# Kernel tuning notes

Hardware: AMD Instinct MI355X
Metric: run time of the kernel (lower is better)

Reference implementation:

```python
import jax, jax.numpy as jnp
import numpy as np

# Dims / scalars (from init_kwargs: m = int(T/dt), delta = dt, theta_star = threshold)
M = 50000
N = 500
DELTA = 0.001
GLEAK = 1.0
TAUS = 10.0
THETA_STAR = 1.0
SPIKE_PROB = 0.02  # sparse binary spike raster as produced by time2spike


def setup_inputs() -> dict:
    key = jax.random.key(0)
    k1, k2, k3 = jax.random.split(key, 3)
    # binary spike raster [m, n]
    spikes = (jax.random.uniform(k1, (M, N)) < SPIKE_PROB).astype(jnp.float32)
    # synapse weights ~ N(w_mean=0.01, 0.01)
    w = (0.01 + 0.01 * jax.random.normal(k2, (N,))).astype(jnp.float32)
    # reversal potentials: half excitatory (ex=5), half inhibitory (inh=-1), shuffled
    vrev = jnp.where(jax.random.uniform(k3, (N,)) < 0.5, 5.0, -1.0).astype(jnp.float32)
    return {"spikes": spikes, "w": w, "vrev": vrev}


def reference(spikes, w, vrev):
    dtype = spikes.dtype
    decay = jnp.exp(jnp.asarray(-1.0 / TAUS, dtype))

    # _compute_exp: exp_temp[i] = (exp_temp[i-1] + spikes[i-1]) * exp(-1/taus), exp_temp[0] = 0
    def exp_step(carry, s):
        nxt = (carry + s) * decay
        return nxt, nxt

    _, e_tail = jax.lax.scan(exp_step, jnp.zeros((N,), dtype), spikes[:-1])
    exp_temp = jnp.concatenate([jnp.zeros((1, N), dtype), e_tail], axis=0)  # [M, N]

    # Gsyn_pre = |w| * exp_temp ; Isyn_pre = Vrev * |w| * exp_temp.
    # Only their per-timestep sums over synapses enter the vtr recurrence,
    # so contract over n immediately instead of materializing [M, N] products.
    absw = jnp.abs(w)
    g_sum = exp_temp @ absw            # [M] = sum_j Gsyn_pre[i, j]
    i_sum = exp_temp @ (vrev * absw)   # [M] = sum_j Isyn_pre[i, j]
    a = DELTA * (GLEAK + g_sum)        # per-step leak+conductance factor
    b = DELTA * i_sum                  # per-step input drive

    # _computevtr: if vtr[i-1] < theta: vtr[i] = vtr[i-1]*(1 - a[i-1]) + b[i-1]
    # else vtr[i] stays 0 (state reset after threshold crossing), vtr[0] = 0.
    def vtr_step(v, ab):
        ai, bi = ab
        nxt = jnp.where(v < THETA_STAR, v * (1.0 - ai) + bi, jnp.asarray(0.0, dtype))
        return nxt, nxt

    _, v_tail = jax.lax.scan(vtr_step, jnp.asarray(0.0, dtype), (a[:-1], b[:-1]))
    vtr = jnp.concatenate([jnp.zeros((1,), dtype), v_tail])  # [M]
    return vtr
```

## Files before the change

kernel.cpp:

```cpp
#include <hip/hip_runtime.h>
#include <cmath>

namespace {
constexpr int NELEM  = 50000;
constexpr int NSYN   = 500;
constexpr int NQ4    = 125;
constexpr int T      = 1024;
constexpr int SBLK   = 49;
constexpr int SLOTS  = SBLK * T;
constexpr int CMAXC  = (NELEM - 1) >> 6;
constexpr int NCH_PAD = 784;
constexpr int MAXSEG = 4096;
constexpr int NGRP   = NELEM / 8;
constexpr double DELTA_D = 1.0e-3;
constexpr double THETA_D = 1.0;
constexpr float  DECAY_F = 0.90483741803595957311f;
}

struct WS {
    double2 rq[SLOTS];
    double  gAm[64], gAg[64], gAi[64];
    double  gPp[64], gPq[64];
    double  gmaxR[1024];
    double  gbndQ[MAXSEG];
    int     gbnd[MAXSEG];
    int     gnseg;
    int     flagA[64];
    int     flagB[64];
    float   swv[SLOTS];
    float   iwv[SLOTS];
};

__device__ inline void pub_d(double* p, double v) {
    __hip_atomic_store(reinterpret_cast<unsigned long long*>(p),
                       __double_as_longlong(v),
                       __ATOMIC_RELAXED, __HIP_MEMORY_SCOPE_AGENT);
}
__device__ inline double rd_d(const double* p) {
    unsigned long long u =
        __hip_atomic_load(reinterpret_cast<const unsigned long long*>(p),
                          __ATOMIC_RELAXED, __HIP_MEMORY_SCOPE_AGENT);
    return __longlong_as_double(u);
}

__global__ __launch_bounds__(256) void k_rowdot(
    const float* __restrict__ spikes,
    const float* __restrict__ w,
    const float* __restrict__ vrev,
    WS* __restrict__ ws)
{
    if (blockIdx.x == 0 && threadIdx.x < 128) {
        const int l = threadIdx.x;
        if (l < 64) ws->flagA[l] = 0; else ws->flagB[l - 64] = 0;
    }

    const int lane = threadIdx.x & 63;
    const int wv   = threadIdx.x >> 6;
    const int rg   = blockIdx.x * 4 + wv;
    if (rg >= NGRP) return;
    const int row0 = rg * 8;

    const float4* __restrict__ w4 = reinterpret_cast<const float4*>(w);
    const float4* __restrict__ r4 = reinterpret_cast<const float4*>(vrev);
    const int j1 = lane;
    const int j2 = lane + 64;
    const bool has2 = (j2 < NQ4);
    float4 a1 = w4[j1], r1 = r4[j1];
    float4 aw1 = make_float4(fabsf(a1.x), fabsf(a1.y), fabsf(a1.z), fabsf(a1.w));
    float4 ar1 = make_float4(aw1.x * r1.x, aw1.y * r1.y, aw1.z * r1.z, aw1.w * r1.w);
    float4 aw2 = make_float4(0.f, 0.f, 0.f, 0.f), ar2 = aw2;
    if (has2) {
        float4 a2 = w4[j2], r2 = r4[j2];
        aw2 = make_float4(fabsf(a2.x), fabsf(a2.y), fabsf(a2.z), fabsf(a2.w));
        ar2 = make_float4(aw2.x * r2.x, aw2.y * r2.y, aw2.z * r2.z, aw2.w * r2.w);
    }

    float sp[8], ip[8];
#pragma unroll
    for (int r = 0; r < 8; ++r) {
        const float4* __restrict__ srow =
            reinterpret_cast<const float4*>(spikes + (size_t)(row0 + r) * NSYN);
        float4 s1 = srow[j1];
        float a = s1.x * aw1.x + s1.y * aw1.y + s1.z * aw1.z + s1.w * aw1.w;
        float b = s1.x * ar1.x + s1.y * ar1.y + s1.z * ar1.z + s1.w * ar1.w;
        if (has2) {
            float4 s2 = srow[j2];
            a += s2.x * aw2.x + s2.y * aw2.y + s2.z * aw2.z + s2.w * aw2.w;
            b += s2.x * ar2.x + s2.y * ar2.y + s2.z * ar2.z + s2.w * ar2.w;
        }
        sp[r] = a; ip[r] = b;
    }
#pragma unroll
    for (int d = 32; d > 0; d >>= 1) {
#pragma unroll
        for (int r = 0; r < 8; ++r) {
            sp[r] += __shfl_xor(sp[r], d);
            ip[r] += __shfl_xor(ip[r], d);
        }
    }
    if (lane == 0) {
        *reinterpret_cast<float4*>(ws->swv + row0)     = make_float4(sp[0], sp[1], sp[2], sp[3]);
        *reinterpret_cast<float4*>(ws->swv + row0 + 4) = make_float4(sp[4], sp[5], sp[6], sp[7]);
        *reinterpret_cast<float4*>(ws->iwv + row0)     = make_float4(ip[0], ip[1], ip[2], ip[3]);
        *reinterpret_cast<float4*>(ws->iwv + row0 + 4) = make_float4(ip[4], ip[5], ip[6], ip[7]);
    }
}

__global__ __launch_bounds__(1024) void k_scan(WS* __restrict__ ws)
{
    const int tid = threadIdx.x, lane = tid & 63, wv = tid >> 6, blk = blockIdx.x;
    const int idx = blk * T + tid;
    const bool live = (idx < NELEM);
    const double decay = (double)DECAY_F;
    __shared__ double s_a[16], s_b[16], s_c[16];
    __shared__ double s_qg0, s_qi0, s_qp0, s_qq0;

    double s = live ? (double)ws->swv[idx] : 0.0;
    double t = live ? (double)ws->iwv[idx] : 0.0;
    double m_in = live ? decay : 1.0;
    double g_in = live ? s * decay : 0.0;
    double i_in = live ? t * decay : 0.0;
#pragma unroll
    for (int d = 1; d < 64; d <<= 1) {
        double pm = __shfl_up(m_in, d);
        double pg = __shfl_up(g_in, d);
        double pi = __shfl_up(i_in, d);
        if (lane >= d) {
            g_in = m_in * pg + g_in;
            i_in = m_in * pi + i_in;
            m_in = pm * m_in;
        }
    }
    if (lane == 63) { s_a[wv] = m_in; s_b[wv] = g_in; s_c[wv] = i_in; }
    __syncthreads();

    if (wv == 0) {
        double wm = (lane < 16) ? s_a[lane] : 1.0;
        double wg = (lane < 16) ? s_b[lane] : 0.0;
        double wi = (lane < 16) ? s_c[lane] : 0.0;
#pragma unroll
        for (int d = 1; d < 16; d <<= 1) {
            double pm = __shfl_up(wm, d);
            double pg = __shfl_up(wg, d);
            double pi = __shfl_up(wi, d);
            if (lane >= d) {
                wg = wm * pg + wg;
                wi = wm * pi + wi;
                wm = pm * wm;
            }
        }
        if (lane < 16) { s_a[lane] = wm; s_b[lane] = wg; s_c[lane] = wi; }
        if (lane == 15) {
            pub_d(&ws->gAm[blk], wm); pub_d(&ws->gAg[blk], wg); pub_d(&ws->gAi[blk], wi);
            __hip_atomic_store(&ws->flagA[blk], 1, __ATOMIC_RELEASE, __HIP_MEMORY_SCOPE_AGENT);
        }
        double am = 1.0, ag = 0.0, ai = 0.0;
        if (lane < SBLK) {
            while (__hip_atomic_load(&ws->flagA[lane], __ATOMIC_ACQUIRE,
                                     __HIP_MEMORY_SCOPE_AGENT) == 0)
                __builtin_amdgcn_s_sleep(1);
            am = rd_d(&ws->gAm[lane]); ag = rd_d(&ws->gAg[lane]); ai = rd_d(&ws->gAi[lane]);
        }
#pragma unroll
        for (int d = 1; d < 64; d <<= 1) {
            double pm = __shfl_up(am, d);
            double pg = __shfl_up(ag, d);
            double pi = __shfl_up(ai, d);
            if (lane >= d) {
                ag = am * pg + ag;
                ai = am * pi + ai;
                am = pm * am;
            }
        }
        double zg = __shfl_up(ag, 1), zi = __shfl_up(ai, 1);
        if (lane == 0) { zg = 0.0; zi = 0.0; }
        if (lane == blk) { s_qg0 = zg; s_qi0 = zi; }
    }
    __syncthreads();

    double em = __shfl_up(m_in, 1), eg = __shfl_up(g_in, 1), ei = __shfl_up(i_in, 1);
    if (lane == 0) { em = 1.0; eg = 0.0; ei = 0.0; }
    if (wv > 0) {
        double qm = s_a[wv - 1], qg = s_b[wv - 1], qi = s_c[wv - 1];
        eg = em * qg + eg;
        ei = em * qi + ei;
        em = qm * em;
    }
    double Eg = em * s_qg0 + eg;
    double Ei = em * s_qi0 + ei;
    double p_in = 1.0, q_in = 0.0;
    if (live) {
        double aa = DELTA_D * (1.0 + Eg);
        double om = 1.0 - aa;
        p_in = om;
        q_in = (DELTA_D * Ei) / om;
    }
    __syncthreads();

#pragma unroll
    for (int d = 1; d < 64; d <<= 1) {
        double pp = __shfl_up(p_in, d);
        double pq = __shfl_up(q_in, d);
        if (lane >= d) {
            q_in = pq + q_in / pp;
            p_in = pp * p_in;
        }
    }
    if (lane == 63) { s_a[wv] = p_in; s_b[wv] = q_in; }
    __syncthreads();

    if (wv == 0) {
        double wp = (lane < 16) ? s_a[lane] : 1.0;
        double wq = (lane < 16) ? s_b[lane] : 0.0;
#pragma unroll
        for (int d = 1; d < 16; d <<= 1) {
            double pp = __shfl_up(wp, d);
            double pq = __shfl_up(wq, d);
            if (lane >= d) {
                wq = pq + wq / pp;
                wp = pp * wp;
            }
        }
        if (lane < 16) { s_a[lane] = wp; s_b[lane] = wq; }
        if (lane == 15) {
            pub_d(&ws->gPp[blk], wp); pub_d(&ws->gPq[blk], wq);
            __hip_atomic_store(&ws->flagB[blk], 1, __ATOMIC_RELEASE, __HIP_MEMORY_SCOPE_AGENT);
        }
        double ap = 1.0, aq = 0.0;
        if (lane < SBLK) {
            while (__hip_atomic_load(&ws->flagB[lane], __ATOMIC_ACQUIRE,
                                     __HIP_MEMORY_SCOPE_AGENT) == 0)
                __builtin_amdgcn_s_sleep(1);
            ap = rd_d(&ws->gPp[lane]); aq = rd_d(&ws->gPq[lane]);
        }
#pragma unroll
        for (int d = 1; d < 64; d <<= 1) {
            double pp = __shfl_up(ap, d);
            double pq = __shfl_up(aq, d);
            if (lane >= d) {
                aq = pq + aq / pp;
                ap = pp * ap;
            }
        }
        double zp = __shfl_up(ap, 1), zq = __shfl_up(aq, 1);
        if (lane == 0) { zp = 1.0; zq = 0.0; }
        if (lane == blk) { s_qp0 = zp; s_qq0 = zq; }
    }
    __syncthreads();

    double ep = __shfl_up(p_in, 1), eq = __shfl_up(q_in, 1);
    if (lane == 0) { ep = 1.0; eq = 0.0; }
    if (wv > 0) {
        double ap2 = s_a[wv - 1], aq2 = s_b[wv - 1];
        eq = aq2 + eq / ap2;
        ep = ap2 * ep;
    }
    double Q = s_qq0 + eq / s_qp0;
    double P = s_qp0 * ep;
    double R = live ? (Q - THETA_D / P) : -1.0e308;
    ws->rq[idx] = make_double2(R, Q);
    double mR = R;
#pragma unroll
    for (int d = 32; d > 0; d >>= 1) mR = fmax(mR, __shfl_xor(mR, d));
    if (lane == 0) ws->gmaxR[idx >> 6] = mR;
}

__global__ __launch_bounds__(1024) void k_search(WS* __restrict__ ws)
{
    const int tid = threadIdx.x, blk = blockIdx.x;

    if (blk == 0) {
        __shared__ double smax[NCH_PAD];
        for (int c = tid; c < NCH_PAD; c += T)
            smax[c] = (c <= CMAXC) ? ws->gmaxR[c] : -1.0e308;
        __syncthreads();

        if (tid < 64) {
            const int lane = tid;
            int nseg = 1;
            if (lane == 0) { ws->gbnd[0] = 0; ws->gbndQ[0] = 0.0; }
            double Qr = 0.0;
            int pos = 1;
            while (pos < NELEM && nseg < MAXSEG) {
                int c = pos >> 6;
                int i0 = -1;
                double Qnb = 0.0;
                while (true) {
                    int cf = -1;
                    for (int cb = c; cb <= CMAXC; cb += 64) {
                        int cc = cb + lane;
                        bool qy = (cc <= CMAXC) && (smax[cc] >= Qr);
                        unsigned long long m = __ballot(qy);
                        if (m) { cf = cb + __builtin_ctzll(m); break; }
                    }
                    if (cf < 0) break;
                    int i = (cf << 6) + lane;
                    bool valid = (i >= pos) && (i < NELEM);
                    double2 rv = valid ? ws->rq[i] : make_double2(-1.0e308, 0.0);
                    unsigned long long m2 = __ballot(valid && (rv.x >= Qr));
                    if (m2) {
                        int r = __builtin_ctzll(m2);
                        i0 = (cf << 6) + r;
                        if (r < 63) Qnb = __shfl(rv.y, r + 1);
                        break;
                    }
                    c = cf + 1;
                    if (c > CMAXC) break;
                }
                if (i0 < 0) break;
                int nb = i0 + 1;
                if (nb >= NELEM) break;
                if ((i0 & 63) == 63) Qnb = ws->rq[nb].y;
                Qr = Qnb;
                if (lane == 0) { ws->gbnd[nseg] = nb; ws->gbndQ[nseg] = Qr; }
                nseg++;
                pos = nb + 1;
            }
            if (lane == 0) ws->gnseg = nseg;
        } else {
            double acc = 0.0;
            for (int i = tid; i < NELEM; i += 7 * T) acc += ws->rq[i].x;
            asm volatile("" :: "v"((float)acc));
        }
    } else if ((blk & 7) == 0) {
        const int p = blk >> 3;
        double acc = 0.0;
        for (int i = p * T + tid; i < NELEM; i += 7 * T) acc += ws->rq[i].x;
        asm volatile("" :: "v"((float)acc));
    }
}

__global__ __launch_bounds__(1024) void k_fill(const WS* __restrict__ ws,
                                               float* __restrict__ out)
{
    __shared__ int    sb[MAXSEG];
    __shared__ double sq[MAXSEG];
    __shared__ int    s_nseg;
    const int tid = threadIdx.x;
    if (tid == 0) s_nseg = ws->gnseg;
    __syncthreads();
    const int nseg = s_nseg;
    for (int i = tid; i < nseg; i += T) { sb[i] = ws->gbnd[i]; sq[i] = ws->gbndQ[i]; }
    __syncthreads();

    const int idx = blockIdx.x * T + tid;
    if (idx < NELEM) {
        int lo = 0, hi = nseg - 1;
        while (lo < hi) {
            int mid = (lo + hi + 1) >> 1;
            if (sb[mid] <= idx) lo = mid; else hi = mid - 1;
        }
        if (idx == sb[lo]) {
            out[idx] = 0.0f;
        } else {
            double2 v = ws->rq[idx];
            double P = THETA_D / (v.y - v.x);
            out[idx] = (float)(P * (v.y - sq[lo]));
        }
    }
}

extern "C" void kernel_launch(void* const* d_in, const int* in_sizes, int n_in,
                              void* d_out, int out_size, void* d_ws, size_t ws_size,
                              hipStream_t stream) {
    const float* spikes = (const float*)d_in[0];
    const float* w      = (const float*)d_in[1];
    const float* vrev   = (const float*)d_in[2];
    float* out = (float*)d_out;
    WS* ws = (WS*)d_ws;

    hipLaunchKernelGGL(k_rowdot, dim3((NGRP + 3) / 4), dim3(256), 0, stream,
                       spikes, w, vrev, ws);
    hipLaunchKernelGGL(k_scan,   dim3(SBLK), dim3(T), 0, stream, ws);
    hipLaunchKernelGGL(k_search, dim3(56),   dim3(T), 0, stream, ws);
    hipLaunchKernelGGL(k_fill,   dim3(SBLK), dim3(T), 0, stream, ws, out);
}
```

Measured before the change: 194.9 us.

## Fuse search and fill kernels into one launch with flag-based handoff

Merges the serial boundary-search kernel and the output fill kernel into a single kernel. Block 0 runs the search and publishes the segment boundaries with atomic stores and a release flag. Blocks 1..49 preload their rq values, then spin on the flag before doing the binary search and writing output. This removes one kernel launch and its inter-kernel gap, and it repartitions the L2-warming prefetch loops into contiguous shares. The spin-wait assumes block 0 is co-resident with the other blocks; 56 blocks of 1024 threads should fit on the device.

```diff
diff --git a/kernel.cpp b/kernel.cpp
--- a/kernel.cpp
+++ b/kernel.cpp
@@ -12,6 +12,7 @@
 constexpr int NCH_PAD = 784;
 constexpr int MAXSEG = 4096;
 constexpr int NGRP   = NELEM / 8;
+constexpr int PSHARE = 7143;
 constexpr double DELTA_D = 1.0e-3;
 constexpr double THETA_D = 1.0;
 constexpr float  DECAY_F = 0.90483741803595957311f;
@@ -27,6 +28,7 @@
     int     gnseg;
     int     flagA[64];
     int     flagB[64];
+    int     flagS;
     float   swv[SLOTS];
     float   iwv[SLOTS];
 };
@@ -41,6 +43,12 @@
         __hip_atomic_load(reinterpret_cast<const unsigned long long*>(p),
                           __ATOMIC_RELAXED, __HIP_MEMORY_SCOPE_AGENT);
     return __longlong_as_double(u);
+}
+__device__ inline void pub_i(int* p, int v) {
+    __hip_atomic_store(p, v, __ATOMIC_RELAXED, __HIP_MEMORY_SCOPE_AGENT);
+}
+__device__ inline int rd_i(const int* p) {
+    return __hip_atomic_load(p, __ATOMIC_RELAXED, __HIP_MEMORY_SCOPE_AGENT);
 }
 
 __global__ __launch_bounds__(256) void k_rowdot(
@@ -49,9 +57,11 @@
     const float* __restrict__ vrev,
     WS* __restrict__ ws)
 {
-    if (blockIdx.x == 0 && threadIdx.x < 128) {
+    if (blockIdx.x == 0 && threadIdx.x < 129) {
         const int l = threadIdx.x;
-        if (l < 64) ws->flagA[l] = 0; else ws->flagB[l - 64] = 0;
+        if (l < 64) ws->flagA[l] = 0;
+        else if (l < 128) ws->flagB[l - 64] = 0;
+        else ws->flagS = 0;
     }
 
     const int lane = threadIdx.x & 63;
@@ -265,12 +275,15 @@
     if (lane == 0) ws->gmaxR[idx >> 6] = mR;
 }
 
-__global__ __launch_bounds__(1024) void k_search(WS* __restrict__ ws)
+__global__ __launch_bounds__(1024) void k_tail(WS* __restrict__ ws, float* __restrict__ out)
 {
     const int tid = threadIdx.x, blk = blockIdx.x;
+    __shared__ double smax[NCH_PAD];
+    __shared__ int    sb[MAXSEG];
+    __shared__ double sq[MAXSEG];
+    __shared__ int    s_nseg;
 
     if (blk == 0) {
-        __shared__ double smax[NCH_PAD];
         for (int c = tid; c < NCH_PAD; c += T)
             smax[c] = (c <= CMAXC) ? ws->gmaxR[c] : -1.0e308;
         __syncthreads();
@@ -278,7 +291,7 @@
         if (tid < 64) {
             const int lane = tid;
             int nseg = 1;
-            if (lane == 0) { ws->gbnd[0] = 0; ws->gbndQ[0] = 0.0; }
+            if (lane == 0) { pub_i(&ws->gbnd[0], 0); pub_d(&ws->gbndQ[0], 0.0); }
             double Qr = 0.0;
             int pos = 1;
             while (pos < NELEM && nseg < MAXSEG) {
@@ -312,39 +325,50 @@
                 if (nb >= NELEM) break;
                 if ((i0 & 63) == 63) Qnb = ws->rq[nb].y;
                 Qr = Qnb;
-                if (lane == 0) { ws->gbnd[nseg] = nb; ws->gbndQ[nseg] = Qr; }
+                if (lane == 0) { pub_i(&ws->gbnd[nseg], nb); pub_d(&ws->gbndQ[nseg], Qr); }
                 nseg++;
                 pos = nb + 1;
             }
-            if (lane == 0) ws->gnseg = nseg;
+            if (lane == 0) {
+                pub_i(&ws->gnseg, nseg);
+                __hip_atomic_store(&ws->flagS, 1, __ATOMIC_RELEASE, __HIP_MEMORY_SCOPE_AGENT);
+            }
         } else {
             double acc = 0.0;
-            for (int i = tid; i < NELEM; i += 7 * T) acc += ws->rq[i].x;
+            for (int i = tid - 64; i < PSHARE; i += 960) acc += ws->rq[i].x;
             asm volatile("" :: "v"((float)acc));
         }
-    } else if ((blk & 7) == 0) {
+        return;
+    }
+    if (blk > SBLK) return;
+
+    const int st = blk - 1;
+    const int idx = st * T + tid;
+    const bool live = (idx < NELEM);
+    double2 v = live ? ws->rq[idx] : make_double2(0.0, 1.0);
+    asm volatile("" :: "v"(v.x), "v"(v.y));
+
+    if ((blk & 7) == 0) {
         const int p = blk >> 3;
+        const int lo = p * PSHARE;
+        const int hi = (lo + PSHARE < NELEM) ? lo + PSHARE : NELEM;
         double acc = 0.0;
-        for (int i = p * T + tid; i < NELEM; i += 7 * T) acc += ws->rq[i].x;
+        for (int i = lo + tid; i < hi; i += T) acc += ws->rq[i].x;
         asm volatile("" :: "v"((float)acc));
     }
-}
-
-__global__ __launch_bounds__(1024) void k_fill(const WS* __restrict__ ws,
-                                               float* __restrict__ out)
-{
-    __shared__ int    sb[MAXSEG];
-    __shared__ double sq[MAXSEG];
-    __shared__ int    s_nseg;
-    const int tid = threadIdx.x;
-    if (tid == 0) s_nseg = ws->gnseg;
+
+    if (tid == 0) {
+        while (__hip_atomic_load(&ws->flagS, __ATOMIC_ACQUIRE,
+                                 __HIP_MEMORY_SCOPE_AGENT) == 0)
+            __builtin_amdgcn_s_sleep(8);
+        s_nseg = rd_i(&ws->gnseg);
+    }
     __syncthreads();
     const int nseg = s_nseg;
-    for (int i = tid; i < nseg; i += T) { sb[i] = ws->gbnd[i]; sq[i] = ws->gbndQ[i]; }
-    __syncthreads();
-
-    const int idx = blockIdx.x * T + tid;
-    if (idx < NELEM) {
+    for (int i = tid; i < nseg; i += T) { sb[i] = rd_i(&ws->gbnd[i]); sq[i] = rd_d(&ws->gbndQ[i]); }
+    __syncthreads();
+
+    if (live) {
         int lo = 0, hi = nseg - 1;
         while (lo < hi) {
             int mid = (lo + hi + 1) >> 1;
@@ -353,7 +377,6 @@
         if (idx == sb[lo]) {
             out[idx] = 0.0f;
         } else {
-            double2 v = ws->rq[idx];
             double P = THETA_D / (v.y - v.x);
             out[idx] = (float)(P * (v.y - sq[lo]));
         }
@@ -372,6 +395,5 @@
     hipLaunchKernelGGL(k_rowdot, dim3((NGRP + 3) / 4), dim3(256), 0, stream,
                        spikes, w, vrev, ws);
     hipLaunchKernelGGL(k_scan,   dim3(SBLK), dim3(T), 0, stream, ws);
-    hipLaunchKernelGGL(k_search, dim3(56),   dim3(T), 0, stream, ws);
-    hipLaunchKernelGGL(k_fill,   dim3(SBLK), dim3(T), 0, stream, ws, out);
-}
+    hipLaunchKernelGGL(k_tail,   dim3(56),   dim3(T), 0, stream, ws, out);
+}
```

Result: slower. 216.9 us (+11.3%).

## Precompute per-element next-reset pointers in parallel, then chase chain serially

Applied to the files above, without the earlier changes.

The serial single-wave threshold search is replaced by a parallel kernel in which every element finds its next reset boundary using a hierarchical max (chunk and group maxima) and stores a (next index, Q) pair. A single thread then follows this pointer chain to emit the segment boundaries, and the L2 warm-up loops now prefetch the new next-pointer array. This takes the per-segment search latency off the serial critical path, at the cost of an extra kernel launch, a new workspace array, and redundant search work for every element.

```diff
diff --git a/kernel.cpp b/kernel.cpp
--- a/kernel.cpp
+++ b/kernel.cpp
@@ -12,6 +12,7 @@
 constexpr int NCH_PAD = 784;
 constexpr int MAXSEG = 4096;
 constexpr int NGRP   = NELEM / 8;
+constexpr int PSH    = 7168;
 constexpr double DELTA_D = 1.0e-3;
 constexpr double THETA_D = 1.0;
 constexpr float  DECAY_F = 0.90483741803595957311f;
@@ -19,6 +20,7 @@
 
 struct WS {
     double2 rq[SLOTS];
+    double2 nxq[SLOTS];
     double  gAm[64], gAg[64], gAi[64];
     double  gPp[64], gPq[64];
     double  gmaxR[1024];
@@ -265,67 +267,92 @@
     if (lane == 0) ws->gmaxR[idx >> 6] = mR;
 }
 
-__global__ __launch_bounds__(1024) void k_search(WS* __restrict__ ws)
+__global__ __launch_bounds__(1024) void k_next(WS* __restrict__ ws)
 {
     const int tid = threadIdx.x, blk = blockIdx.x;
+    const int idx = blk * T + tid;
+    const bool live = (idx < NELEM);
+    __shared__ double sR[T];
+    __shared__ double smax[NCH_PAD];
+    __shared__ double sgmax[64];
+
+    double2 v = ws->rq[idx];
+    sR[tid] = v.x;
+    if (tid < NCH_PAD)
+        smax[tid] = (tid <= CMAXC) ? ws->gmaxR[tid] : -1.0e308;
+    __syncthreads();
+    if (tid < SBLK) {
+        double g = -1.0e308;
+        for (int c = tid * 16; c < tid * 16 + 16; ++c) g = fmax(g, smax[c]);
+        sgmax[tid] = g;
+    }
+    __syncthreads();
+
+    int nb = NELEM;
+    if (live && idx + 1 < NELEM) {
+        const double thr = v.y;
+        const int myc = tid >> 6;
+        int i0 = -1;
+        const int lcend = (myc << 6) + 64;
+        for (int t2 = tid + 1; t2 < lcend; ++t2)
+            if (sR[t2] >= thr) { i0 = blk * T + t2; break; }
+        if (i0 < 0) {
+            for (int c = myc + 1; c < 16; ++c) {
+                if (smax[(blk << 4) + c] >= thr) {
+                    for (int t2 = c << 6; t2 < (c << 6) + 64; ++t2)
+                        if (sR[t2] >= thr) { i0 = blk * T + t2; break; }
+                    break;
+                }
+            }
+        }
+        if (i0 < 0) {
+            for (int g = blk + 1; g < SBLK; ++g) {
+                if (sgmax[g] >= thr) {
+                    int ch = -1;
+                    for (int c = g << 4; c < (g << 4) + 16; ++c)
+                        if (smax[c] >= thr) { ch = c; break; }
+                    const int b0 = ch << 6;
+                    for (int k = 0; k < 64; ++k)
+                        if (ws->rq[b0 + k].x >= thr) { i0 = b0 + k; break; }
+                    break;
+                }
+            }
+        }
+        if (i0 >= 0 && i0 + 1 < NELEM) nb = i0 + 1;
+    }
+    double Qn = (nb < NELEM) ? ws->rq[nb].y : 0.0;
+    ws->nxq[idx] = make_double2((double)nb, Qn);
+}
+
+__global__ __launch_bounds__(1024) void k_chain(WS* __restrict__ ws)
+{
+    const int tid = threadIdx.x, blk = blockIdx.x;
 
     if (blk == 0) {
-        __shared__ double smax[NCH_PAD];
-        for (int c = tid; c < NCH_PAD; c += T)
-            smax[c] = (c <= CMAXC) ? ws->gmaxR[c] : -1.0e308;
-        __syncthreads();
-
-        if (tid < 64) {
-            const int lane = tid;
+        if (tid == 0) {
+            ws->gbnd[0] = 0; ws->gbndQ[0] = 0.0;
             int nseg = 1;
-            if (lane == 0) { ws->gbnd[0] = 0; ws->gbndQ[0] = 0.0; }
-            double Qr = 0.0;
-            int pos = 1;
-            while (pos < NELEM && nseg < MAXSEG) {
-                int c = pos >> 6;
-                int i0 = -1;
-                double Qnb = 0.0;
-                while (true) {
-                    int cf = -1;
-                    for (int cb = c; cb <= CMAXC; cb += 64) {
-                        int cc = cb + lane;
-                        bool qy = (cc <= CMAXC) && (smax[cc] >= Qr);
-                        unsigned long long m = __ballot(qy);
-                        if (m) { cf = cb + __builtin_ctzll(m); break; }
-                    }
-                    if (cf < 0) break;
-                    int i = (cf << 6) + lane;
-                    bool valid = (i >= pos) && (i < NELEM);
-                    double2 rv = valid ? ws->rq[i] : make_double2(-1.0e308, 0.0);
-                    unsigned long long m2 = __ballot(valid && (rv.x >= Qr));
-                    if (m2) {
-                        int r = __builtin_ctzll(m2);
-                        i0 = (cf << 6) + r;
-                        if (r < 63) Qnb = __shfl(rv.y, r + 1);
-                        break;
-                    }
-                    c = cf + 1;
-                    if (c > CMAXC) break;
-                }
-                if (i0 < 0) break;
-                int nb = i0 + 1;
+            int b = 0;
+            while (nseg < MAXSEG) {
+                double2 v = ws->nxq[b];
+                int nb = (int)v.x;
                 if (nb >= NELEM) break;
-                if ((i0 & 63) == 63) Qnb = ws->rq[nb].y;
-                Qr = Qnb;
-                if (lane == 0) { ws->gbnd[nseg] = nb; ws->gbndQ[nseg] = Qr; }
+                ws->gbnd[nseg] = nb; ws->gbndQ[nseg] = v.y;
                 nseg++;
-                pos = nb + 1;
-            }
-            if (lane == 0) ws->gnseg = nseg;
-        } else {
+                b = nb;
+            }
+            ws->gnseg = nseg;
+        } else if (tid >= 64) {
             double acc = 0.0;
-            for (int i = tid; i < NELEM; i += 7 * T) acc += ws->rq[i].x;
+            for (int i = tid - 64; i < PSH; i += 960) acc += ws->nxq[i].x;
             asm volatile("" :: "v"((float)acc));
         }
     } else if ((blk & 7) == 0) {
         const int p = blk >> 3;
+        const int lo = p * PSH;
+        const int hi = (lo + PSH < SLOTS) ? lo + PSH : SLOTS;
         double acc = 0.0;
-        for (int i = p * T + tid; i < NELEM; i += 7 * T) acc += ws->rq[i].x;
+        for (int i = lo + tid; i < hi; i += T) acc += ws->nxq[i].x;
         asm volatile("" :: "v"((float)acc));
     }
 }
@@ -371,7 +398,8 @@
 
     hipLaunchKernelGGL(k_rowdot, dim3((NGRP + 3) / 4), dim3(256), 0, stream,
                        spikes, w, vrev, ws);
-    hipLaunchKernelGGL(k_scan,   dim3(SBLK), dim3(T), 0, stream, ws);
-    hipLaunchKernelGGL(k_search, dim3(56),   dim3(T), 0, stream, ws);
-    hipLaunchKernelGGL(k_fill,   dim3(SBLK), dim3(T), 0, stream, ws, out);
-}
+    hipLaunchKernelGGL(k_scan,  dim3(SBLK), dim3(T), 0, stream, ws);
+    hipLaunchKernelGGL(k_next,  dim3(SBLK), dim3(T), 0, stream, ws);
+    hipLaunchKernelGGL(k_chain, dim3(56),   dim3(T), 0, stream, ws);
+    hipLaunchKernelGGL(k_fill,  dim3(SBLK), dim3(T), 0, stream, ws, out);
+}
```

Measured after the change: 208.2 us. +6.8%, slower.
